# Kernel optimization log

Hardware: AMD Instinct MI355X
Metric: run time of the kernel (lower is better)

## Reference

```python
import jax, jax.numpy as jnp
import numpy as np
from jax import lax

EMB, HID, L, PATCH, IMG, K = 192, 64, 6, 4, 224, 8
FMAP = IMG // PATCH
N = FMAP * FMAP
B = 8
ALG = 4
GB_np = np.array([0, 1, 1, 2])  # grade of each blade [1, e1, e2, e12]
GB = jnp.asarray(GB_np)

def _cayley_np():
    C = np.zeros((4, 4, 4), np.float32)
    tbl = {(0,0):(0,1.),(0,1):(1,1.),(0,2):(2,1.),(0,3):(3,1.),
           (1,0):(1,1.),(1,1):(0,1.),(1,2):(3,1.),(1,3):(2,1.),
           (2,0):(2,1.),(2,1):(3,-1.),(2,2):(0,1.),(2,3):(1,-1.),
           (3,0):(3,1.),(3,1):(2,-1.),(3,2):(1,1.),(3,3):(0,-1.)}
    for (i, j), (k, s) in tbl.items():
        C[i, j, k] = s
    return C

CAY_np = _cayley_np()
CAYLEY = jnp.asarray(CAY_np)
_paths = np.zeros((3, 3, 3), bool)
for _i in range(4):
    for _j in range(4):
        for _k in range(4):
            if CAY_np[_i, _j, _k] != 0:
                _paths[GB_np[_i], GB_np[_j], GB_np[_k]] = True
PI, PJ, PK = (jnp.asarray(a) for a in np.nonzero(_paths))
NPATH = int(_paths.sum())  # 10 geometric-product paths for Cl(2,0)

def build_knn_graph(H, W, k):
    yy, xx = np.meshgrid(np.arange(H, dtype=np.float32), np.arange(W, dtype=np.float32), indexing='ij')
    coords = np.stack([xx.ravel(), yy.ravel()], -1)
    cn = coords / np.array([W - 1, H - 1], np.float32) * 2 - 1
    d = np.linalg.norm(cn[:, None] - cn[None], axis=-1)
    np.fill_diagonal(d, np.inf)
    idx = np.argsort(d, axis=-1, kind='stable')[:, :k]
    rows = np.repeat(np.arange(H * W), k)
    cols = idx.reshape(-1)
    return rows.astype(np.int32), cols.astype(np.int32), cn.astype(np.float32)

def mvlin(x, W, b=None):
    # per-grade MVLinear: W [out,in,3] expanded to blades via GB
    y = jnp.einsum('nmi,bmi->bni', W[:, :, GB], x)
    if b is not None:
        y = y.at[:, :, 0].add(b)  # bias embedded in scalar blade only
    return y

def mvlin_flat(x, W, b):
    # subspaces=False MVLinear: same weight across blades
    y = jnp.einsum('nm,bmi->bni', W, x)
    return y.at[:, :, 0].add(b)

def mv_silu(x, a, b):
    # invariants: [scalar, q(grade1), q(grade2)]; gate = sigmoid(a*inv+b)
    inv = jnp.concatenate([x[..., :1], x[..., 1:2]**2 + x[..., 2:3]**2, x[..., 3:4]**2], -1)
    return jax.nn.sigmoid(a * inv + b)[..., GB] * x

def normalize_mv(x, a):
    q = jnp.concatenate([x[..., :1]**2, x[..., 1:2]**2 + x[..., 2:3]**2, x[..., 3:4]**2], -1)
    n = jnp.sqrt(q + 1e-12)
    d = jax.nn.sigmoid(a) * (n - 1.0) + 1.0
    return x / (d + 1e-6)[..., GB]

def sgp(x, Wl, bl, Wr, na, gw):
    # SteerableGeometricProductLayer
    xr = normalize_mv(mvlin(x, Wr), na)
    full = jnp.zeros((gw.shape[0], 3, 3, 3), x.dtype).at[:, PI, PJ, PK].set(gw)
    fb = full[:, GB][:, :, GB][:, :, :, GB]  # [feat,4,4,4]
    gp = jnp.einsum('bni,nijk,bnk->bnj', x, CAYLEY[None] * fb, xr)
    return (mvlin(x, Wl, bl) + gp) * np.float32(1.0 / np.sqrt(2.0))

def _forward(x, conv_w, conv_b, stem_g, stem_b, pos_embed, in_W, in_b, in_Wl, in_bl, in_Wr, in_na, in_gw, eg_eW, eg_eb, eg_sa, eg_sb, eg_nW, eg_nb, eg_Wl, eg_bl, eg_Wr, eg_na, eg_gw, eg_aa, eg_ab, out_W, out_b, on_g, on_b, cls_W, cls_b, coords, rows, cols):
    Bx = x.shape[0]
    # stem: strided conv + LayerNorm over (C,H,W)
    y = lax.conv_general_dilated(x, conv_w, (PATCH, PATCH), 'VALID', dimension_numbers=('NCHW', 'OIHW', 'NCHW')) + conv_b[None, :, None, None]
    mu = y.mean(axis=(1, 2, 3), keepdims=True)
    var = ((y - mu) ** 2).mean(axis=(1, 2, 3), keepdims=True)
    y = (y - mu) / jnp.sqrt(var + 1e-5) * stem_g[None] + stem_b[None]
    y = y + pos_embed
    feat = y.transpose(0, 2, 3, 1).reshape(Bx * N, EMB)
    # embed features in scalar blade, coordinates in vector blades e1,e2
    h = jnp.zeros((Bx * N, EMB + 1, ALG), x.dtype)
    h = h.at[:, :EMB, 0].set(feat)
    h = h.at[:, EMB, 1:3].set(jnp.tile(coords, (Bx, 1)))
    h = sgp(mvlin_flat(h, in_W, in_b), in_Wl, in_bl, in_Wr, in_na, in_gw)
    BN = Bx * N
    for i in range(L):
        m = mv_silu(mvlin(h[rows] - h[cols], eg_eW[i], eg_eb[i]), eg_sa[i], eg_sb[i])
        agg = jax.ops.segment_sum(m, rows, num_segments=BN)  # count computed but unused in original
        nu = mvlin(jnp.concatenate([h, agg], axis=1), eg_nW[i], eg_nb[i])
        out = mv_silu(sgp(nu, eg_Wl[i], eg_bl[i], eg_Wr[i], eg_na[i], eg_gw[i]), eg_aa[i], eg_ab[i])
        h = h + out if i > 0 else out
    s = mvlin_flat(h, out_W, out_b)[..., 0]
    mu2 = s.mean(-1, keepdims=True)
    v2 = ((s - mu2) ** 2).mean(-1, keepdims=True)
    s = (s - mu2) / jnp.sqrt(v2 + 1e-5) * on_g + on_b
    pooled = s.reshape(Bx, N, EMB).mean(axis=1)
    return pooled @ cls_W.T + cls_b

def setup_inputs() -> dict:
    key = jax.random.key(0)
    ks = iter(jax.random.split(key, 64))
    nrm = lambda shape, s=0.05: jax.random.normal(next(ks), shape, jnp.float32) * s
    rows, cols, cn = build_knn_graph(FMAP, FMAP, K)
    offs = np.arange(B, dtype=np.int32)[:, None] * N
    rows_b = (rows[None] + offs).reshape(-1)
    cols_b = (cols[None] + offs).reshape(-1)
    return dict(
        x=jax.random.normal(next(ks), (B, 3, IMG, IMG), jnp.float32),
        conv_w=nrm((EMB, 3, PATCH, PATCH)),
        conv_b=jnp.zeros((EMB,), jnp.float32),
        stem_g=jnp.ones((EMB, FMAP, FMAP), jnp.float32),
        stem_b=jnp.zeros((EMB, FMAP, FMAP), jnp.float32),
        pos_embed=nrm((1, EMB, FMAP, FMAP), 0.02),
        coords=jnp.asarray(cn),
        in_W=nrm((HID, EMB + 1)), in_b=jnp.zeros((HID,), jnp.float32),
        in_Wl=nrm((HID, HID, 3)), in_bl=jnp.zeros((HID,), jnp.float32),
        in_Wr=nrm((HID, HID, 3)), in_na=jnp.zeros((HID, 3), jnp.float32),
        in_gw=nrm((HID, NPATH), 0.2),
        eg_eW=nrm((L, HID, HID, 3)), eg_eb=jnp.zeros((L, HID), jnp.float32),
        eg_sa=jnp.ones((L, HID, 3), jnp.float32), eg_sb=jnp.zeros((L, HID, 3), jnp.float32),
        eg_nW=nrm((L, HID, 2 * HID, 3)), eg_nb=jnp.zeros((L, HID), jnp.float32),
        eg_Wl=nrm((L, HID, HID, 3)), eg_bl=jnp.zeros((L, HID), jnp.float32),
        eg_Wr=nrm((L, HID, HID, 3)), eg_na=jnp.zeros((L, HID, 3), jnp.float32),
        eg_gw=nrm((L, HID, NPATH), 0.2),
        eg_aa=jnp.ones((L, HID, 3), jnp.float32), eg_ab=jnp.zeros((L, HID, 3), jnp.float32),
        out_W=nrm((EMB, HID)), out_b=jnp.zeros((EMB,), jnp.float32),
        on_g=jnp.ones((EMB,), jnp.float32), on_b=jnp.zeros((EMB,), jnp.float32),
        cls_W=nrm((10, EMB), 0.02), cls_b=jnp.zeros((10,), jnp.float32),
        rows=jnp.asarray(rows_b), cols=jnp.asarray(cols_b),
    )

def reference(x, conv_w, conv_b, stem_g, stem_b, pos_embed, coords, in_W, in_b, in_Wl, in_bl, in_Wr, in_na, in_gw, eg_eW, eg_eb, eg_sa, eg_sb, eg_nW, eg_nb, eg_Wl, eg_bl, eg_Wr, eg_na, eg_gw, eg_aa, eg_ab, out_W, out_b, on_g, on_b, cls_W, cls_b, rows, cols):
    return _forward(x, conv_w, conv_b, stem_g, stem_b, pos_embed, in_W, in_b, in_Wl, in_bl, in_Wr, in_na, in_gw, eg_eW, eg_eb, eg_sa, eg_sb, eg_nW, eg_nb, eg_Wl, eg_bl, eg_Wr, eg_na, eg_gw, eg_aa, eg_ab, out_W, out_b, on_g, on_b, cls_W, cls_b, coords, rows, cols)
```

## Files before the change

kernel.cpp:

```cpp
#include <hip/hip_runtime.h>
#include <hip/hip_bf16.h>
#include <math.h>

#define EMBC   192
#define NLAY   6
#define IMGC   224
#define FMAPC  56
#define NNODE  3136
#define NBATCH 8
#define BNODES 25088
#define KNNE   8
#define NT     32
#define RSQRT2 0.70710678118654752f

typedef float f4v __attribute__((ext_vector_type(4)));

__device__ __forceinline__ float sigm(float x){ return 1.0f/(1.0f+__expf(-x)); }
__device__ __forceinline__ f4v ntld(const float* p){
  return __builtin_nontemporal_load((const f4v*)p);
}
__device__ __forceinline__ void ntst(float* p, f4v v){
  __builtin_nontemporal_store(v, (f4v*)p);
}

__global__ void k_repackw(const float* __restrict__ src, float* __restrict__ dst, int K){
  int l = blockIdx.y;
  size_t S = (size_t)64*K*3;
  int t = blockIdx.x*256 + threadIdx.x;
  if(t < (int)S){
    int j = t % 3; int r = t / 3;
    int ci = r % 8; int m = (r / 8) % K; int wid = r / (8*K);
    dst[l*S + (((size_t)wid*K + m)*8 + ci)*3 + j] =
      src[l*S + ((size_t)(wid*8+ci)*K + m)*3 + j];
  }
}
__global__ void k_repack1(const float* __restrict__ src, float* __restrict__ dst,
                          int R, int K){
  int t = blockIdx.x*256 + threadIdx.x;
  if(t < R*K){
    int m = t % K, r = t / K;
    dst[m*R + r] = src[r*K + m];
  }
}

__global__ void k_tr(const float* __restrict__ g, const float* __restrict__ sb,
                     const float* __restrict__ pe, float* __restrict__ g2,
                     float* __restrict__ pb2){
  int n = blockIdx.x; int c = threadIdx.x;
  g2[n*EMBC + c]  = g[c*NNODE + n];
  pb2[n*EMBC + c] = sb[c*NNODE + n] + pe[c*NNODE + n];
}

__global__ __launch_bounds__(256) void k_conv(const float* __restrict__ x,
    const float* __restrict__ cw, const float* __restrict__ cb,
    float* __restrict__ y0, float* __restrict__ parts){
  __shared__ float xs[2688];
  __shared__ float wsh[9216];
  __shared__ float red[512];
  int blk = blockIdx.x; int b = blk / FMAPC; int ph = blk % FMAPC;
  int tid = threadIdx.x;
  for(int t = tid; t < 9216; t += 256) wsh[t] = cw[t];
  for(int t = tid; t < 2688; t += 256){
    int r = t / IMGC; int w = t % IMGC;
    int ci = r >> 2, kh = r & 3;
    xs[t] = x[((size_t)(b*3 + ci)*IMGC + (ph*4 + kh))*IMGC + w];
  }
  __syncthreads();
  float s1 = 0.f, s2 = 0.f;
  for(int oi = tid; oi < FMAPC*EMBC; oi += 256){
    int pw = oi / EMBC; int c = oi % EMBC;
    float acc = cb[c];
    const float4* wv4 = (const float4*)(wsh + c*48);
    #pragma unroll
    for(int r = 0; r < 12; ++r){
      float4 xv = *((const float4*)(xs + r*IMGC + pw*4));
      float4 wv = wv4[r];
      acc += xv.x*wv.x + xv.y*wv.y + xv.z*wv.z + xv.w*wv.w;
    }
    y0[((size_t)(b*NNODE + ph*FMAPC + pw))*EMBC + c] = acc;
    s1 += acc; s2 += acc*acc;
  }
  red[tid] = s1; red[256+tid] = s2;
  __syncthreads();
  for(int st = 128; st > 0; st >>= 1){
    if(tid < st){ red[tid] += red[tid+st]; red[256+tid] += red[256+tid+st]; }
    __syncthreads();
  }
  if(tid == 0){ parts[blk*2] = red[0]; parts[blk*2+1] = red[256]; }
}

__global__ void k_stats(const float* __restrict__ parts, float* __restrict__ stats){
  int b = threadIdx.x;
  if(b < NBATCH){
    float S = 0.f, Q = 0.f;
    for(int j = 0; j < FMAPC; ++j){ S += parts[(b*FMAPC+j)*2]; Q += parts[(b*FMAPC+j)*2+1]; }
    float cnt = (float)(EMBC*NNODE);
    float mu = S/cnt;
    float var = Q/cnt - mu*mu;
    stats[b*2] = mu; stats[b*2+1] = rsqrtf(var + 1e-5f);
  }
}

__global__ __launch_bounds__(256,2) void k_embed(const float* __restrict__ y0,
    const float* __restrict__ stats, const float* __restrict__ g2,
    const float* __restrict__ pb2, const float* __restrict__ inWp,
    const float* __restrict__ inb, const float* __restrict__ coords,
    float* __restrict__ xmv){
  __shared__ float fs[64*193];
  int tid = threadIdx.x, lane = tid & 63;
  int wid = __builtin_amdgcn_readfirstlane(tid >> 6);
  int ch0 = wid << 4;
  int p0 = blockIdx.x * 64;
  int b = p0 / NNODE; int n0 = p0 - b*NNODE;
  float mu = stats[b*2], rstd = stats[b*2+1];
  for(int t = tid; t < 64*192; t += 256){
    int n = t / 192, c = t - n*192;
    int nn = n0 + n;
    fs[n*193 + c] = (y0[(size_t)(p0+n)*192 + c] - mu)*rstd*g2[nn*192+c] + pb2[nn*192+c];
  }
  __syncthreads();
  float acc[16];
  #pragma unroll
  for(int ci = 0; ci < 16; ++ci) acc[ci] = 0.f;
  #pragma unroll 2
  for(int m = 0; m < 192; ++m){
    float xm = fs[lane*193 + m];
    const float* wp = inWp + m*64 + ch0;
    #pragma unroll
    for(int ci = 0; ci < 16; ++ci) acc[ci] += wp[ci]*xm;
  }
  float cx = coords[(n0+lane)*2], cy = coords[(n0+lane)*2+1];
  #pragma unroll
  for(int ci = 0; ci < 16; ++ci){
    int ch = ch0 + ci;
    float wc = inWp[192*64 + ch];
    float4 v; v.x = acc[ci] + inb[ch]; v.y = wc*cx; v.z = wc*cy; v.w = 0.f;
    *((float4*)(xmv + ((size_t)(p0+lane)*64 + ch)*4)) = v;
  }
}

__device__ __forceinline__ void stage_x(float* xs, const float* __restrict__ g,
                                        int p0, int tid){
  #pragma unroll
  for(int t = tid; t < NT*64; t += 512){
    int n = t >> 6, m = t & 63;
    f4v v = ntld(g + (((size_t)(p0+n))<<8) + (m<<2));
    *((f4v*)(xs + (n<<8) + (((m + n)&63)<<2))) = v;
  }
}
__device__ __forceinline__ void copyout(const float* xs, float* __restrict__ g,
                                        int p0, int tid){
  #pragma unroll
  for(int t = tid; t < NT*64; t += 512){
    int n = t >> 6, m = t & 63;
    f4v v = *((const f4v*)(xs + (n<<8) + (((m + n)&63)<<2)));
    ntst(g + (((size_t)(p0+n))<<8) + (m<<2), v);
  }
}
__device__ __forceinline__ void stage_w(float* wst, const float* __restrict__ Wp,
                                        int K, int moff, int tid){
  #pragma unroll
  for(int t = tid; t < 3072; t += 512){
    int c = t / 384, r = t - c*384;
    ((float4*)wst)[t] = ((const float4*)(Wp + ((size_t)(c*K + moff)*24)))[r];
  }
}
__device__ __forceinline__ void stage_wh(float* wst, int dstoff,
                                         const float* __restrict__ Wp,
                                         int K, int moff, int tid){
  #pragma unroll
  for(int t = tid; t < 1536; t += 512){
    int c = t / 192, r = t - c*192;
    ((float4*)(wst + dstoff))[c*192 + r] =
      ((const float4*)(Wp + ((size_t)(c*K + moff)*24)))[r];
  }
}
__device__ __forceinline__ void mm4(float (&acc)[4][4], const float* __restrict__ wst,
                                    const float* __restrict__ xrow, int wb, int n){
  #pragma unroll 4
  for(int m = 0; m < 64; ++m){
    float4 xv = *((const float4*)(xrow + (((m + n)&63)<<2)));
    const float* wp = wst + wb + m*24;
    float4 a = *((const float4*)wp);
    float4 b = *((const float4*)(wp+4));
    float4 c = *((const float4*)(wp+8));
    acc[0][0]+=a.x*xv.x; acc[0][1]+=a.y*xv.y; acc[0][2]+=a.y*xv.z; acc[0][3]+=a.z*xv.w;
    acc[1][0]+=a.w*xv.x; acc[1][1]+=b.x*xv.y; acc[1][2]+=b.x*xv.z; acc[1][3]+=b.y*xv.w;
    acc[2][0]+=b.z*xv.x; acc[2][1]+=b.w*xv.y; acc[2][2]+=b.w*xv.z; acc[2][3]+=c.x*xv.w;
    acc[3][0]+=c.y*xv.x; acc[3][1]+=c.z*xv.y; acc[3][2]+=c.z*xv.z; acc[3][3]+=c.w*xv.w;
  }
}
__device__ __forceinline__ void mm4f(float (&p)[4][4], float (&q)[4][4],
    const float* __restrict__ wst, const float* __restrict__ xrow,
    int wbA, int wbB, int n, int mg0){
  #pragma unroll 4
  for(int m = 0; m < 32; ++m){
    float4 xv = *((const float4*)(xrow + (((m + mg0 + n)&63)<<2)));
    const float* wa = wst + wbA + m*24;
    const float* wb_ = wst + wbB + m*24;
    float4 a = *((const float4*)wa);
    float4 b = *((const float4*)(wa+4));
    float4 c = *((const float4*)(wa+8));
    p[0][0]+=a.x*xv.x; p[0][1]+=a.y*xv.y; p[0][2]+=a.y*xv.z; p[0][3]+=a.z*xv.w;
    p[1][0]+=a.w*xv.x; p[1][1]+=b.x*xv.y; p[1][2]+=b.x*xv.z; p[1][3]+=b.y*xv.w;
    p[2][0]+=b.z*xv.x; p[2][1]+=b.w*xv.y; p[2][2]+=b.w*xv.z; p[2][3]+=c.x*xv.w;
    p[3][0]+=c.y*xv.x; p[3][1]+=c.z*xv.y; p[3][2]+=c.z*xv.z; p[3][3]+=c.w*xv.w;
    float4 d = *((const float4*)wb_);
    float4 e = *((const float4*)(wb_+4));
    float4 f = *((const float4*)(wb_+8));
    q[0][0]+=d.x*xv.x; q[0][1]+=d.y*xv.y; q[0][2]+=d.y*xv.z; q[0][3]+=d.z*xv.w;
    q[1][0]+=d.w*xv.x; q[1][1]+=e.x*xv.y; q[1][2]+=e.x*xv.z; q[1][3]+=e.y*xv.w;
    q[2][0]+=e.z*xv.x; q[2][1]+=e.w*xv.y; q[2][2]+=e.w*xv.z; q[2][3]+=f.x*xv.w;
    q[3][0]+=f.y*xv.x; q[3][1]+=f.z*xv.y; q[3][2]+=f.z*xv.z; q[3][3]+=f.w*xv.w;
  }
}
#define ZERO44(A) { _Pragma("unroll") for(int _i=0;_i<4;++_i) _Pragma("unroll") for(int _j=0;_j<4;++_j) A[_i][_j]=0.f; }

__global__ __launch_bounds__(512,4) void k_sgp0(const float* __restrict__ src,
    float* __restrict__ h, float* __restrict__ zout,
    const float* __restrict__ Wlp, const float* __restrict__ bl,
    const float* __restrict__ Wrp, const float* __restrict__ na,
    const float* __restrict__ gw, const float* __restrict__ zWp){
  __shared__ float xs[NT*256];
  __shared__ float wst[12288];
  int tid = threadIdx.x, lane = tid & 63;
  int wid = __builtin_amdgcn_readfirstlane(tid >> 6);
  int n = lane & 31, s = lane >> 5;
  int ch0 = (wid<<3) + s*4;
  int wb  = wid*1536 + s*12;
  int wbA = wid*768 + s*12, wbB = 6144 + wbA;
  int p0 = blockIdx.x * NT;
  const float* xrow = xs + (n<<8);
  stage_x(xs, src, p0, tid);
  stage_wh(wst, 0, Wlp, 64, 0, tid);
  stage_wh(wst, 6144, Wrp, 64, 0, tid);
  __syncthreads();
  float accl[4][4], accr[4][4];
  ZERO44(accl); ZERO44(accr);
  mm4f(accl, accr, wst, xrow, wbA, wbB, n, 0);
  __syncthreads();
  stage_wh(wst, 0, Wlp, 64, 32, tid);
  stage_wh(wst, 6144, Wrp, 64, 32, tid);
  __syncthreads();
  mm4f(accl, accr, wst, xrow, wbA, wbB, n, 32);
  float out[4][4];
  #pragma unroll
  for(int ci = 0; ci < 4; ++ci){
    int ch = ch0 + ci;
    float yr0 = accr[ci][0], yr1 = accr[ci][1], yr2 = accr[ci][2], yr3 = accr[ci][3];
    float na0 = sigm(na[ch*3]), na1 = sigm(na[ch*3+1]), na2 = sigm(na[ch*3+2]);
    float d0 = na0*(sqrtf(yr0*yr0 + 1e-12f) - 1.f) + 1.f + 1e-6f;
    float d1 = na1*(sqrtf(yr1*yr1 + yr2*yr2 + 1e-12f) - 1.f) + 1.f + 1e-6f;
    float d2 = na2*(sqrtf(yr3*yr3 + 1e-12f) - 1.f) + 1.f + 1e-6f;
    float xq0 = yr0/d0, xq1 = yr1/d1, xq2 = yr2/d1, xq3 = yr3/d2;
    float4 xv = *((const float4*)(xrow + (((ch + n)&63)<<2)));
    const float* gwp = gw + ch*10;
    float gp0 = gwp[0]*xv.x*xq0 + gwp[3]*(xv.y*xq1 + xv.z*xq2) + gwp[7]*xv.w*xq3;
    float gp1 = gwp[1]*xv.x*xq1 + gwp[4]*xv.y*xq0 - gwp[5]*xv.z*xq3 - gwp[8]*xv.w*xq2;
    float gp2 = gwp[1]*xv.x*xq2 + gwp[4]*xv.z*xq0 + gwp[5]*xv.y*xq3 + gwp[8]*xv.w*xq1;
    float gp3 = gwp[2]*xv.x*xq3 + gwp[6]*(xv.y*xq2 - xv.z*xq1) - gwp[9]*xv.w*xq0;
    out[ci][0] = (accl[ci][0] + bl[ch] + gp0)*RSQRT2;
    out[ci][1] = (accl[ci][1] + gp1)*RSQRT2;
    out[ci][2] = (accl[ci][2] + gp2)*RSQRT2;
    out[ci][3] = (accl[ci][3] + gp3)*RSQRT2;
  }
  __syncthreads();
  #pragma unroll
  for(int ci = 0; ci < 4; ++ci){
    int ch = ch0 + ci;
    float4 v; v.x=out[ci][0]; v.y=out[ci][1]; v.z=out[ci][2]; v.w=out[ci][3];
    *((float4*)(xs + (n<<8) + (((ch + n)&63)<<2))) = v;
  }
  __syncthreads();
  copyout(xs, h, p0, tid);
  stage_w(wst, zWp, 64, 0, tid);
  __syncthreads();
  float zA[4][4];
  ZERO44(zA);
  mm4(zA, wst, xrow, wb, n);
  __syncthreads();
  #pragma unroll
  for(int ci = 0; ci < 4; ++ci){
    int ch = ch0 + ci;
    float4 v; v.x=zA[ci][0]; v.y=zA[ci][1]; v.z=zA[ci][2]; v.w=zA[ci][3];
    *((float4*)(xs + (n<<8) + (((ch + n)&63)<<2))) = v;
  }
  __syncthreads();
  copyout(xs, zout, p0, tid);
}

__global__ __launch_bounds__(512,4) void k_layer(
    float* __restrict__ h, const float* __restrict__ z,
    float* __restrict__ zout, const int* __restrict__ cols,
    const float* __restrict__ eb, const float* __restrict__ sa,
    const float* __restrict__ sb,
    const float* __restrict__ nWp, const float* __restrict__ nb,
    const float* __restrict__ Wlp, const float* __restrict__ bl,
    const float* __restrict__ Wrp, const float* __restrict__ na,
    const float* __restrict__ gw, const float* __restrict__ aa,
    const float* __restrict__ ab,
    const float* __restrict__ zWp, int mode){
  __shared__ float xs[NT*256];
  __shared__ float wst[12288];
  int tid = threadIdx.x, lane = tid & 63;
  int wid = __builtin_amdgcn_readfirstlane(tid >> 6);
  int n = lane & 31, s = lane >> 5;
  int ch0 = (wid<<3) + s*4;
  int wb  = wid*1536 + s*12;
  int wbA = wid*768 + s*12, wbB = 6144 + wbA;
  int p0 = blockIdx.x * NT;
  const float* xrow = xs + (n<<8);
  float ag[4][4];
  {
    int ch = lane;
    float ebv = eb[ch];
    float a0 = sa[ch*3], a1 = sa[ch*3+1], a2 = sa[ch*3+2];
    float b0 = sb[ch*3], b1 = sb[ch*3+1], b2 = sb[ch*3+2];
    #pragma unroll
    for(int e = 0; e < 4; ++e){
      int p = p0 + wid*4 + e;
      float4 zo = *((const float4*)(z + ((size_t)p*64 + ch)*4));
      float ax=0.f, ay=0.f, az_=0.f, aw=0.f;
      #pragma unroll
      for(int k = 0; k < KNNE; ++k){
        int c = cols[p*KNNE + k];
        float4 zc = *((const float4*)(z + ((size_t)c*64 + ch)*4));
        float d0 = zo.x - zc.x + ebv;
        float d1 = zo.y - zc.y;
        float d2 = zo.z - zc.z;
        float d3 = zo.w - zc.w;
        float g0 = sigm(a0*d0 + b0);
        float g1 = sigm(a1*(d1*d1 + d2*d2) + b1);
        float g2v = sigm(a2*(d3*d3) + b2);
        ax += g0*d0; ay += g1*d1; az_ += g1*d2; aw += g2v*d3;
      }
      ag[e][0]=ax; ag[e][1]=ay; ag[e][2]=az_; ag[e][3]=aw;
    }
  }
  stage_x(xs, h, p0, tid);
  stage_w(wst, nWp, 128, 0, tid);
  __syncthreads();
  float nuA[4][4];
  ZERO44(nuA);
  mm4(nuA, wst, xrow, wb, n);
  float hrA[4][4];
  if(mode == 2){
    #pragma unroll
    for(int ci = 0; ci < 4; ++ci){
      int ch = ch0 + ci;
      float4 v0 = *((const float4*)(xrow + (((ch + n)&63)<<2)));
      hrA[ci][0]=v0.x; hrA[ci][1]=v0.y; hrA[ci][2]=v0.z; hrA[ci][3]=v0.w;
    }
  }
  __syncthreads();
  #pragma unroll
  for(int e = 0; e < 4; ++e){
    int nn = wid*4 + e;
    float4 v; v.x=ag[e][0]; v.y=ag[e][1]; v.z=ag[e][2]; v.w=ag[e][3];
    *((float4*)(xs + (nn<<8) + (((lane + nn)&63)<<2))) = v;
  }
  stage_w(wst, nWp, 128, 64, tid);
  __syncthreads();
  mm4(nuA, wst, xrow, wb, n);
  __syncthreads();
  #pragma unroll
  for(int ci = 0; ci < 4; ++ci){
    int ch = ch0 + ci;
    nuA[ci][0] += nb[ch];
    float4 v; v.x=nuA[ci][0]; v.y=nuA[ci][1]; v.z=nuA[ci][2]; v.w=nuA[ci][3];
    *((float4*)(xs + (n<<8) + (((ch + n)&63)<<2))) = v;
  }
  stage_wh(wst, 0, Wlp, 64, 0, tid);
  stage_wh(wst, 6144, Wrp, 64, 0, tid);
  __syncthreads();
  float accl[4][4], accr[4][4];
  ZERO44(accl); ZERO44(accr);
  mm4f(accl, accr, wst, xrow, wbA, wbB, n, 0);
  __syncthreads();
  stage_wh(wst, 0, Wlp, 64, 32, tid);
  stage_wh(wst, 6144, Wrp, 64, 32, tid);
  __syncthreads();
  mm4f(accl, accr, wst, xrow, wbA, wbB, n, 32);
  float out[4][4];
  #pragma unroll
  for(int ci = 0; ci < 4; ++ci){
    int ch = ch0 + ci;
    float yr0 = accr[ci][0], yr1 = accr[ci][1], yr2 = accr[ci][2], yr3 = accr[ci][3];
    float na0 = sigm(na[ch*3]), na1 = sigm(na[ch*3+1]), na2 = sigm(na[ch*3+2]);
    float d0 = na0*(sqrtf(yr0*yr0 + 1e-12f) - 1.f) + 1.f + 1e-6f;
    float d1 = na1*(sqrtf(yr1*yr1 + yr2*yr2 + 1e-12f) - 1.f) + 1.f + 1e-6f;
    float d2 = na2*(sqrtf(yr3*yr3 + 1e-12f) - 1.f) + 1.f + 1e-6f;
    float xq0 = yr0/d0, xq1 = yr1/d1, xq2 = yr2/d1, xq3 = yr3/d2;
    float x0 = nuA[ci][0], x1 = nuA[ci][1], x2 = nuA[ci][2], x3 = nuA[ci][3];
    const float* gwp = gw + ch*10;
    float gp0 = gwp[0]*x0*xq0 + gwp[3]*(x1*xq1 + x2*xq2) + gwp[7]*x3*xq3;
    float gp1 = gwp[1]*x0*xq1 + gwp[4]*x1*xq0 - gwp[5]*x2*xq3 - gwp[8]*x3*xq2;
    float gp2 = gwp[1]*x0*xq2 + gwp[4]*x2*xq0 + gwp[5]*x1*xq3 + gwp[8]*x3*xq1;
    float gp3 = gwp[2]*x0*xq3 + gwp[6]*(x1*xq2 - x2*xq1) - gwp[9]*x3*xq0;
    float o0 = (accl[ci][0] + bl[ch] + gp0)*RSQRT2;
    float o1 = (accl[ci][1] + gp1)*RSQRT2;
    float o2 = (accl[ci][2] + gp2)*RSQRT2;
    float o3 = (accl[ci][3] + gp3)*RSQRT2;
    float g0 = sigm(aa[ch*3]*o0 + ab[ch*3]);
    float g1 = sigm(aa[ch*3+1]*(o1*o1 + o2*o2) + ab[ch*3+1]);
    float g2v = sigm(aa[ch*3+2]*(o3*o3) + ab[ch*3+2]);
    float v0 = g0*o0, v1 = g1*o1, v2 = g1*o2, v3 = g2v*o3;
    if(mode == 2){ v0 += hrA[ci][0]; v1 += hrA[ci][1]; v2 += hrA[ci][2]; v3 += hrA[ci][3]; }
    out[ci][0]=v0; out[ci][1]=v1; out[ci][2]=v2; out[ci][3]=v3;
  }
  __syncthreads();
  #pragma unroll
  for(int ci = 0; ci < 4; ++ci){
    int ch = ch0 + ci;
    float4 v; v.x=out[ci][0]; v.y=out[ci][1]; v.z=out[ci][2]; v.w=out[ci][3];
    *((float4*)(xs + (n<<8) + (((ch + n)&63)<<2))) = v;
  }
  __syncthreads();
  copyout(xs, h, p0, tid);
  if(zWp != nullptr){
    stage_w(wst, zWp, 64, 0, tid);
    __syncthreads();
    float zA[4][4];
    ZERO44(zA);
    mm4(zA, wst, xrow, wb, n);
    __syncthreads();
    #pragma unroll
    for(int ci = 0; ci < 4; ++ci){
      int ch = ch0 + ci;
      float4 v; v.x=zA[ci][0]; v.y=zA[ci][1]; v.z=zA[ci][2]; v.w=zA[ci][3];
      *((float4*)(xs + (n<<8) + (((ch + n)&63)<<2))) = v;
    }
    __syncthreads();
    copyout(xs, zout, p0, tid);
  }
}

__global__ __launch_bounds__(256,2) void k_head(const float* __restrict__ h,
    const float* __restrict__ oWp, const float* __restrict__ ob,
    const float* __restrict__ ong, const float* __restrict__ onb,
    float* __restrict__ s){
  __shared__ float hs[64*65];
  __shared__ float rr[512];
  int tid = threadIdx.x, lane = tid & 63;
  int wid = __builtin_amdgcn_readfirstlane(tid >> 6);
  int c0 = wid*48;
  int p0 = blockIdx.x * 64;
  for(int t = tid; t < 64*64; t += 256){
    int nn = t >> 6, c = t & 63;
    hs[nn*65 + c] = h[(((size_t)(p0+nn))*64 + c)*4];
  }
  __syncthreads();
  float a[48];
  #pragma unroll
  for(int ci = 0; ci < 48; ++ci) a[ci] = 0.f;
  #pragma unroll 2
  for(int m = 0; m < 64; ++m){
    float xm = hs[lane*65 + m];
    const float* wp = oWp + m*192 + c0;
    #pragma unroll
    for(int ci = 0; ci < 48; ++ci) a[ci] += wp[ci]*xm;
  }
  float s1 = 0.f, s2 = 0.f;
  #pragma unroll
  for(int ci = 0; ci < 48; ++ci){
    a[ci] += ob[c0+ci];
    s1 += a[ci]; s2 += a[ci]*a[ci];
  }
  rr[wid*64 + lane] = s1; rr[256 + wid*64 + lane] = s2;
  __syncthreads();
  float S = rr[lane] + rr[64+lane] + rr[128+lane] + rr[192+lane];
  float Q = rr[256+lane] + rr[320+lane] + rr[384+lane] + rr[448+lane];
  float mu = S*(1.0f/EMBC);
  float var = Q*(1.0f/EMBC) - mu*mu;
  float rstd = rsqrtf(var + 1e-5f);
  #pragma unroll
  for(int q = 0; q < 12; ++q){
    int c = c0 + q*4;
    float4 v;
    v.x = (a[q*4  ] - mu)*rstd*ong[c  ] + onb[c  ];
    v.y = (a[q*4+1] - mu)*rstd*ong[c+1] + onb[c+1];
    v.z = (a[q*4+2] - mu)*rstd*ong[c+2] + onb[c+2];
    v.w = (a[q*4+3] - mu)*rstd*ong[c+3] + onb[c+3];
    *((float4*)(s + (size_t)(p0+lane)*192 + c)) = v;
  }
}

__global__ void k_pool1(const float* __restrict__ s, float* __restrict__ pp){
  int blk = blockIdx.x;
  int b = blk >> 5, chunk = blk & 31;
  int c = threadIdx.x;
  float acc = 0.f;
  int n0 = chunk*98;
  for(int j = 0; j < 98; ++j) acc += s[((size_t)(b*NNODE + n0 + j))*EMBC + c];
  pp[(size_t)blk*EMBC + c] = acc;
}
__global__ void k_pool2(const float* __restrict__ pp, float* __restrict__ pooled){
  int b = blockIdx.x; int c = threadIdx.x;
  float acc = 0.f;
  for(int j = 0; j < 32; ++j) acc += pp[((size_t)(b*32 + j))*EMBC + c];
  pooled[b*EMBC + c] = acc * (1.0f/NNODE);
}

__global__ void k_cls(const float* __restrict__ pooled, const float* __restrict__ cW,
                      const float* __restrict__ cb, float* __restrict__ out){
  int tid = threadIdx.x;
  if(tid < NBATCH*10){
    int b = tid/10, k = tid%10;
    float acc = cb[k];
    for(int c = 0; c < EMBC; ++c) acc += pooled[b*EMBC + c]*cW[k*EMBC + c];
    out[tid] = acc;
  }
}

extern "C" void kernel_launch(void* const* d_in, const int* in_sizes, int n_in,
                              void* d_out, int out_size, void* d_ws, size_t ws_size,
                              hipStream_t stream){
  const float* x      = (const float*)d_in[0];
  const float* conv_w = (const float*)d_in[1];
  const float* conv_b = (const float*)d_in[2];
  const float* stem_g = (const float*)d_in[3];
  const float* stem_b = (const float*)d_in[4];
  const float* pos_e  = (const float*)d_in[5];
  const float* coords = (const float*)d_in[6];
  const float* inW    = (const float*)d_in[7];
  const float* inb    = (const float*)d_in[8];
  const float* inWl   = (const float*)d_in[9];
  const float* inbl   = (const float*)d_in[10];
  const float* inWr   = (const float*)d_in[11];
  const float* inna   = (const float*)d_in[12];
  const float* ingw   = (const float*)d_in[13];
  const float* eg_eW  = (const float*)d_in[14];
  const float* eg_eb  = (const float*)d_in[15];
  const float* eg_sa  = (const float*)d_in[16];
  const float* eg_sb  = (const float*)d_in[17];
  const float* eg_nW  = (const float*)d_in[18];
  const float* eg_nb  = (const float*)d_in[19];
  const float* eg_Wl  = (const float*)d_in[20];
  const float* eg_bl  = (const float*)d_in[21];
  const float* eg_Wr  = (const float*)d_in[22];
  const float* eg_na  = (const float*)d_in[23];
  const float* eg_gw  = (const float*)d_in[24];
  const float* eg_aa  = (const float*)d_in[25];
  const float* eg_ab  = (const float*)d_in[26];
  const float* outW   = (const float*)d_in[27];
  const float* outb   = (const float*)d_in[28];
  const float* ong    = (const float*)d_in[29];
  const float* onb    = (const float*)d_in[30];
  const float* clsW   = (const float*)d_in[31];
  const float* clsb   = (const float*)d_in[32];
  const int*   cols   = (const int*)d_in[34];

  float* ws = (float*)d_ws;
  size_t off = 0;
  float* hbuf  = ws + off; off += (size_t)BNODES*256;
  float* bigA  = ws + off; off += (size_t)BNODES*256;
  float* bigB  = ws + off; off += (size_t)BNODES*256;
  float* g2    = ws + off; off += (size_t)NNODE*EMBC;
  float* pb2   = ws + off; off += (size_t)NNODE*EMBC;
  float* parts = ws + off; off += 896;
  float* stats = ws + off; off += 16;
  float* pp    = ws + off; off += 256*EMBC;
  float* pooled= ws + off; off += NBATCH*EMBC;
  float* wpInW = ws + off; off += 193*64;
  float* wpOW  = ws + off; off += 64*192;
  float* wpInWl= ws + off; off += 12288;
  float* wpInWr= ws + off; off += 12288;
  float* wpEW  = ws + off; off += (size_t)NLAY*12288;
  float* wpWl  = ws + off; off += (size_t)NLAY*12288;
  float* wpWr  = ws + off; off += (size_t)NLAY*12288;
  float* wpNW  = ws + off; off += (size_t)NLAY*24576;
  float* y0    = bigB;

  const int NTILE = BNODES/NT;

  { dim3 g1((12352+255)/256); k_repack1<<<g1, 256, 0, stream>>>(inW,  wpInW, 64, 193); }
  { dim3 g1((12288+255)/256); k_repack1<<<g1, 256, 0, stream>>>(outW, wpOW, 192, 64); }
  { dim3 g3((12288+255)/256, 1); k_repackw<<<g3, 256, 0, stream>>>(inWl, wpInWl, 64); }
  { dim3 g3((12288+255)/256, 1); k_repackw<<<g3, 256, 0, stream>>>(inWr, wpInWr, 64); }
  { dim3 g3((12288+255)/256, NLAY); k_repackw<<<g3, 256, 0, stream>>>(eg_eW, wpEW, 64); }
  { dim3 g3((12288+255)/256, NLAY); k_repackw<<<g3, 256, 0, stream>>>(eg_Wl, wpWl, 64); }
  { dim3 g3((12288+255)/256, NLAY); k_repackw<<<g3, 256, 0, stream>>>(eg_Wr, wpWr, 64); }
  { dim3 g3((24576+255)/256, NLAY); k_repackw<<<g3, 256, 0, stream>>>(eg_nW, wpNW, 128); }

  k_tr   <<<NNODE, 192, 0, stream>>>(stem_g, stem_b, pos_e, g2, pb2);
  k_conv <<<NBATCH*FMAPC, 256, 0, stream>>>(x, conv_w, conv_b, y0, parts);
  k_stats<<<1, 64, 0, stream>>>(parts, stats);
  k_embed<<<BNODES/64, 256, 0, stream>>>(y0, stats, g2, pb2, wpInW, inb, coords, bigA);
  k_sgp0 <<<NTILE, 512, 0, stream>>>(bigA, hbuf, bigB, wpInWl, inbl, wpInWr,
                                     inna, ingw, wpEW);
  float* zcur = bigB;
  float* spare = bigA;
  for(int l = 0; l < NLAY; ++l){
    const float* zWn = (l < NLAY-1) ? (wpEW + (size_t)(l+1)*12288) : (const float*)nullptr;
    k_layer<<<NTILE, 512, 0, stream>>>(hbuf, zcur, spare, cols,
        eg_eb + l*64, eg_sa + l*192, eg_sb + l*192,
        wpNW + (size_t)l*24576, eg_nb + l*64,
        wpWl + (size_t)l*12288, eg_bl + l*64,
        wpWr + (size_t)l*12288, eg_na + l*192,
        eg_gw + l*640, eg_aa + l*192, eg_ab + l*192,
        zWn, (l==0)?1:2);
    if(l < NLAY-1){ float* t = zcur; zcur = spare; spare = t; }
  }
  k_head <<<BNODES/64, 256, 0, stream>>>(hbuf, wpOW, outb, ong, onb, spare);
  k_pool1<<<256, 192, 0, stream>>>(spare, pp);
  k_pool2<<<8, 192, 0, stream>>>(pp, pooled);
  k_cls  <<<1, 128, 0, stream>>>(pooled, clsW, clsb, (float*)d_out);
}
```

Baseline: 1.581 ms.

## Prefetch next weight tile into registers during matmul, remap block order

Replaces the synchronous shared-memory weight staging, previously split into Wl/Wr halves, with full 64-row tiles. The next tile (Wr, zW, second nW half) is loaded into registers while the current matmul runs, then written to shared memory after a barrier. This hides global load latency behind compute. Block indices are remapped with an (bid&7)*stride + bid>>3 swizzle, likely to spread consecutive blocks across XCDs for cache locality. Nontemporal loads and stores are replaced by plain ones. The prefetch uses more registers, which may reduce occupancy under launch_bounds(512,4).

```diff
diff --git a/kernel.cpp b/kernel.cpp
--- a/kernel.cpp
+++ b/kernel.cpp
@@ -13,15 +13,7 @@
 #define NT     32
 #define RSQRT2 0.70710678118654752f
 
-typedef float f4v __attribute__((ext_vector_type(4)));
-
 __device__ __forceinline__ float sigm(float x){ return 1.0f/(1.0f+__expf(-x)); }
-__device__ __forceinline__ f4v ntld(const float* p){
-  return __builtin_nontemporal_load((const f4v*)p);
-}
-__device__ __forceinline__ void ntst(float* p, f4v v){
-  __builtin_nontemporal_store(v, (f4v*)p);
-}
 
 __global__ void k_repackw(const float* __restrict__ src, float* __restrict__ dst, int K){
   int l = blockIdx.y;
@@ -110,7 +102,9 @@
   int tid = threadIdx.x, lane = tid & 63;
   int wid = __builtin_amdgcn_readfirstlane(tid >> 6);
   int ch0 = wid << 4;
-  int p0 = blockIdx.x * 64;
+  int bid = blockIdx.x;
+  int blk = (bid & 7)*49 + (bid >> 3);
+  int p0 = blk * 64;
   int b = p0 / NNODE; int n0 = p0 - b*NNODE;
   float mu = stats[b*2], rstd = stats[b*2+1];
   for(int t = tid; t < 64*192; t += 256){
@@ -139,41 +133,45 @@
   }
 }
 
-__device__ __forceinline__ void stage_x(float* xs, const float* __restrict__ g,
+__device__ __forceinline__ void xload(float4 (&r)[4], const float* __restrict__ g,
+                                      int p0, int tid){
+  #pragma unroll
+  for(int i = 0; i < 4; ++i){
+    int t = tid + i*512;
+    int nn = t >> 6, m = t & 63;
+    r[i] = *((const float4*)(g + (((size_t)(p0+nn))<<8) + (m<<2)));
+  }
+}
+__device__ __forceinline__ void xwrite(float* xs, const float4 (&r)[4], int tid){
+  #pragma unroll
+  for(int i = 0; i < 4; ++i){
+    int t = tid + i*512;
+    int nn = t >> 6, m = t & 63;
+    *((float4*)(xs + (nn<<8) + (((m + nn)&63)<<2))) = r[i];
+  }
+}
+__device__ __forceinline__ void copyout(const float* xs, float* __restrict__ g,
                                         int p0, int tid){
   #pragma unroll
   for(int t = tid; t < NT*64; t += 512){
     int n = t >> 6, m = t & 63;
-    f4v v = ntld(g + (((size_t)(p0+n))<<8) + (m<<2));
-    *((f4v*)(xs + (n<<8) + (((m + n)&63)<<2))) = v;
-  }
-}
-__device__ __forceinline__ void copyout(const float* xs, float* __restrict__ g,
-                                        int p0, int tid){
-  #pragma unroll
-  for(int t = tid; t < NT*64; t += 512){
-    int n = t >> 6, m = t & 63;
-    f4v v = *((const f4v*)(xs + (n<<8) + (((m + n)&63)<<2)));
-    ntst(g + (((size_t)(p0+n))<<8) + (m<<2), v);
-  }
-}
-__device__ __forceinline__ void stage_w(float* wst, const float* __restrict__ Wp,
-                                        int K, int moff, int tid){
-  #pragma unroll
-  for(int t = tid; t < 3072; t += 512){
-    int c = t / 384, r = t - c*384;
-    ((float4*)wst)[t] = ((const float4*)(Wp + ((size_t)(c*K + moff)*24)))[r];
-  }
-}
-__device__ __forceinline__ void stage_wh(float* wst, int dstoff,
-                                         const float* __restrict__ Wp,
-                                         int K, int moff, int tid){
-  #pragma unroll
-  for(int t = tid; t < 1536; t += 512){
-    int c = t / 192, r = t - c*192;
-    ((float4*)(wst + dstoff))[c*192 + r] =
-      ((const float4*)(Wp + ((size_t)(c*K + moff)*24)))[r];
-  }
+    float4 v = *((const float4*)(xs + (n<<8) + (((m + n)&63)<<2)));
+    *((float4*)(g + (((size_t)(p0+n))<<8) + (m<<2))) = v;
+  }
+}
+__device__ __forceinline__ void wload(float4 (&r)[6], const float* __restrict__ Wp,
+                                      int K, int moff, int tid){
+  #pragma unroll
+  for(int i = 0; i < 6; ++i){
+    int t = tid + i*512;
+    int c = t / 384, q = t - c*384;
+    r[i] = ((const float4*)(Wp + ((size_t)(c*K + moff)*24)))[q];
+  }
+}
+__device__ __forceinline__ void wwrite(float* wst, const float4 (&r)[6], int tid){
+  #pragma unroll
+  for(int i = 0; i < 6; ++i)
+    ((float4*)wst)[tid + i*512] = r[i];
 }
 __device__ __forceinline__ void mm4(float (&acc)[4][4], const float* __restrict__ wst,
                                     const float* __restrict__ xrow, int wb, int n){
@@ -190,30 +188,6 @@
     acc[3][0]+=c.y*xv.x; acc[3][1]+=c.z*xv.y; acc[3][2]+=c.z*xv.z; acc[3][3]+=c.w*xv.w;
   }
 }
-__device__ __forceinline__ void mm4f(float (&p)[4][4], float (&q)[4][4],
-    const float* __restrict__ wst, const float* __restrict__ xrow,
-    int wbA, int wbB, int n, int mg0){
-  #pragma unroll 4
-  for(int m = 0; m < 32; ++m){
-    float4 xv = *((const float4*)(xrow + (((m + mg0 + n)&63)<<2)));
-    const float* wa = wst + wbA + m*24;
-    const float* wb_ = wst + wbB + m*24;
-    float4 a = *((const float4*)wa);
-    float4 b = *((const float4*)(wa+4));
-    float4 c = *((const float4*)(wa+8));
-    p[0][0]+=a.x*xv.x; p[0][1]+=a.y*xv.y; p[0][2]+=a.y*xv.z; p[0][3]+=a.z*xv.w;
-    p[1][0]+=a.w*xv.x; p[1][1]+=b.x*xv.y; p[1][2]+=b.x*xv.z; p[1][3]+=b.y*xv.w;
-    p[2][0]+=b.z*xv.x; p[2][1]+=b.w*xv.y; p[2][2]+=b.w*xv.z; p[2][3]+=c.x*xv.w;
-    p[3][0]+=c.y*xv.x; p[3][1]+=c.z*xv.y; p[3][2]+=c.z*xv.z; p[3][3]+=c.w*xv.w;
-    float4 d = *((const float4*)wb_);
-    float4 e = *((const float4*)(wb_+4));
-    float4 f = *((const float4*)(wb_+8));
-    q[0][0]+=d.x*xv.x; q[0][1]+=d.y*xv.y; q[0][2]+=d.y*xv.z; q[0][3]+=d.z*xv.w;
-    q[1][0]+=d.w*xv.x; q[1][1]+=e.x*xv.y; q[1][2]+=e.x*xv.z; q[1][3]+=e.y*xv.w;
-    q[2][0]+=e.z*xv.x; q[2][1]+=e.w*xv.y; q[2][2]+=e.w*xv.z; q[2][3]+=f.x*xv.w;
-    q[3][0]+=f.y*xv.x; q[3][1]+=f.z*xv.y; q[3][2]+=f.z*xv.z; q[3][3]+=f.w*xv.w;
-  }
-}
 #define ZERO44(A) { _Pragma("unroll") for(int _i=0;_i<4;++_i) _Pragma("unroll") for(int _j=0;_j<4;++_j) A[_i][_j]=0.f; }
 
 __global__ __launch_bounds__(512,4) void k_sgp0(const float* __restrict__ src,
@@ -228,21 +202,25 @@
   int n = lane & 31, s = lane >> 5;
   int ch0 = (wid<<3) + s*4;
   int wb  = wid*1536 + s*12;
-  int wbA = wid*768 + s*12, wbB = 6144 + wbA;
-  int p0 = blockIdx.x * NT;
+  int bid = blockIdx.x;
+  int blk = (bid & 7)*98 + (bid >> 3);
+  int p0 = blk * NT;
   const float* xrow = xs + (n<<8);
-  stage_x(xs, src, p0, tid);
-  stage_wh(wst, 0, Wlp, 64, 0, tid);
-  stage_wh(wst, 6144, Wrp, 64, 0, tid);
-  __syncthreads();
+  float4 wr_[6]; float4 xr_[4];
+  wload(wr_, Wlp, 64, 0, tid);
+  xload(xr_, src, p0, tid);
+  wwrite(wst, wr_, tid);
+  xwrite(xs, xr_, tid);
+  __syncthreads();
+  wload(wr_, Wrp, 64, 0, tid);
   float accl[4][4], accr[4][4];
   ZERO44(accl); ZERO44(accr);
-  mm4f(accl, accr, wst, xrow, wbA, wbB, n, 0);
-  __syncthreads();
-  stage_wh(wst, 0, Wlp, 64, 32, tid);
-  stage_wh(wst, 6144, Wrp, 64, 32, tid);
-  __syncthreads();
-  mm4f(accl, accr, wst, xrow, wbA, wbB, n, 32);
+  mm4(accl, wst, xrow, wb, n);
+  __syncthreads();
+  wwrite(wst, wr_, tid);
+  __syncthreads();
+  wload(wr_, zWp, 64, 0, tid);
+  mm4(accr, wst, xrow, wb, n);
   float out[4][4];
   #pragma unroll
   for(int ci = 0; ci < 4; ++ci){
@@ -273,7 +251,7 @@
   }
   __syncthreads();
   copyout(xs, h, p0, tid);
-  stage_w(wst, zWp, 64, 0, tid);
+  wwrite(wst, wr_, tid);
   __syncthreads();
   float zA[4][4];
   ZERO44(zA);
@@ -307,9 +285,13 @@
   int n = lane & 31, s = lane >> 5;
   int ch0 = (wid<<3) + s*4;
   int wb  = wid*1536 + s*12;
-  int wbA = wid*768 + s*12, wbB = 6144 + wbA;
-  int p0 = blockIdx.x * NT;
+  int bid = blockIdx.x;
+  int blk = (bid & 7)*98 + (bid >> 3);
+  int p0 = blk * NT;
   const float* xrow = xs + (n<<8);
+  float4 wr_[6]; float4 xr_[4];
+  wload(wr_, nWp, 128, 0, tid);
+  xload(xr_, h, p0, tid);
   float ag[4][4];
   {
     int ch = lane;
@@ -337,9 +319,10 @@
       ag[e][0]=ax; ag[e][1]=ay; ag[e][2]=az_; ag[e][3]=aw;
     }
   }
-  stage_x(xs, h, p0, tid);
-  stage_w(wst, nWp, 128, 0, tid);
-  __syncthreads();
+  wwrite(wst, wr_, tid);
+  xwrite(xs, xr_, tid);
+  __syncthreads();
+  wload(wr_, nWp, 128, 64, tid);
   float nuA[4][4];
   ZERO44(nuA);
   mm4(nuA, wst, xrow, wb, n);
@@ -359,8 +342,9 @@
     float4 v; v.x=ag[e][0]; v.y=ag[e][1]; v.z=ag[e][2]; v.w=ag[e][3];
     *((float4*)(xs + (nn<<8) + (((lane + nn)&63)<<2))) = v;
   }
-  stage_w(wst, nWp, 128, 64, tid);
-  __syncthreads();
+  wwrite(wst, wr_, tid);
+  __syncthreads();
+  wload(wr_, Wlp, 64, 0, tid);
   mm4(nuA, wst, xrow, wb, n);
   __syncthreads();
   #pragma unroll
@@ -370,17 +354,17 @@
     float4 v; v.x=nuA[ci][0]; v.y=nuA[ci][1]; v.z=nuA[ci][2]; v.w=nuA[ci][3];
     *((float4*)(xs + (n<<8) + (((ch + n)&63)<<2))) = v;
   }
-  stage_wh(wst, 0, Wlp, 64, 0, tid);
-  stage_wh(wst, 6144, Wrp, 64, 0, tid);
-  __syncthreads();
+  wwrite(wst, wr_, tid);
+  __syncthreads();
+  wload(wr_, Wrp, 64, 0, tid);
   float accl[4][4], accr[4][4];
   ZERO44(accl); ZERO44(accr);
-  mm4f(accl, accr, wst, xrow, wbA, wbB, n, 0);
-  __syncthreads();
-  stage_wh(wst, 0, Wlp, 64, 32, tid);
-  stage_wh(wst, 6144, Wrp, 64, 32, tid);
-  __syncthreads();
-  mm4f(accl, accr, wst, xrow, wbA, wbB, n, 32);
+  mm4(accl, wst, xrow, wb, n);
+  __syncthreads();
+  wwrite(wst, wr_, tid);
+  __syncthreads();
+  if(zWp != nullptr) wload(wr_, zWp, 64, 0, tid);
+  mm4(accr, wst, xrow, wb, n);
   float out[4][4];
   #pragma unroll
   for(int ci = 0; ci < 4; ++ci){
@@ -418,7 +402,7 @@
   __syncthreads();
   copyout(xs, h, p0, tid);
   if(zWp != nullptr){
-    stage_w(wst, zWp, 64, 0, tid);
+    wwrite(wst, wr_, tid);
     __syncthreads();
     float zA[4][4];
     ZERO44(zA);
@@ -444,7 +428,9 @@
   int tid = threadIdx.x, lane = tid & 63;
   int wid = __builtin_amdgcn_readfirstlane(tid >> 6);
   int c0 = wid*48;
-  int p0 = blockIdx.x * 64;
+  int bid = blockIdx.x;
+  int blk = (bid & 7)*49 + (bid >> 3);
+  int p0 = blk * 64;
   for(int t = tid; t < 64*64; t += 256){
     int nn = t >> 6, c = t & 63;
     hs[nn*65 + c] = h[(((size_t)(p0+nn))*64 + c)*4];
```

Result: slower. 2.849 ms (+80.2%).
